# Kernel optimization log

Hardware: AMD Instinct MI355X
Metric: run time of the kernel (lower is better)

The kernel has to match this reference:

```python
import jax, jax.numpy as jnp
import numpy as np
import math

B, N, WIDTH, HEADS = 2, 2048, 1024, 16
ATTN_CH = WIDTH // HEADS  # 64 (note: width//heads//3 of the 3*width fused dim)


def setup_inputs() -> dict:
    key = jax.random.key(0)
    ks = jax.random.split(key, 3)
    std = 0.02
    return {
        "x": jax.random.normal(ks[0], (B, N, WIDTH), dtype=jnp.float32),
        "w_qkv": jax.random.normal(ks[1], (WIDTH, 3 * WIDTH), dtype=jnp.float32) * std,
        "b_qkv": jnp.zeros((3 * WIDTH,), dtype=jnp.float32),
        "w_proj": jax.random.normal(ks[2], (WIDTH, WIDTH), dtype=jnp.float32) * std,
        "b_proj": jnp.zeros((WIDTH,), dtype=jnp.float32),
    }


def reference(x, w_qkv, b_qkv, w_proj, b_proj):
    bs, n_ctx, width = x.shape
    qkv = x @ w_qkv + b_qkv                       # [b, n, 3*width]
    attn_ch = (3 * width) // HEADS // 3           # head dim
    scale = 1.0 / math.sqrt(math.sqrt(attn_ch))
    # per-head layout: [b, n, heads, 3*attn_ch] -> split q,k,v
    qkv = qkv.reshape(bs, n_ctx, HEADS, 3 * attn_ch)
    q, k, v = jnp.split(qkv, 3, axis=-1)          # each [b, n, h, c]
    weight = jnp.einsum("bthc,bshc->bhts", q * scale, k * scale)
    weight = jax.nn.softmax(weight.astype(jnp.float32), axis=-1).astype(qkv.dtype)
    out = jnp.einsum("bhts,bshc->bthc", weight, v).reshape(bs, n_ctx, -1)
    return out @ w_proj + b_proj
```

## Files before the change

### kernel.cpp

```cpp
#include <hip/hip_runtime.h>
#include <hip/hip_fp16.h>

#define BATCH 2
#define NCTX  2048
#define WIDTH 1024
#define HEADS 16
#define CH    64
#define QKVD  (3 * WIDTH)
#define MROWS (BATCH * NCTX)

typedef __attribute__((ext_vector_type(4))) float    f32x4;
typedef __attribute__((ext_vector_type(8))) _Float16 f16x8;
typedef __attribute__((ext_vector_type(4))) _Float16 f16x4;

#define QSCALE 0.18033688011112042f

__device__ __forceinline__ unsigned pkrtz(float a, float b) {
    auto p = __builtin_amdgcn_cvt_pkrtz(a, b);
    return __builtin_bit_cast(unsigned, p);
}

__global__ __launch_bounds__(256)
void split_x_f16(const float* __restrict__ x, __half* __restrict__ tiles)
{
    const int mb = blockIdx.x, kt = blockIdx.y;
    const int t = threadIdx.x;
    __half* tb = (__half*)tiles + ((size_t)mb * 32 + kt) * 4096;
    #pragma unroll
    for (int it = 0; it < 2; ++it) {
        const int idx = it * 256 + t;
        const int m = idx >> 2, q = idx & 3;
        const float* src = x + (size_t)(mb * 128 + m) * WIDTH + kt * 32 + q * 8;
        const f32x4 v0 = *(const f32x4*)src;
        const f32x4 v1 = *(const f32x4*)(src + 4);
        f16x8 h;
        #pragma unroll
        for (int j = 0; j < 4; ++j) { h[j] = (_Float16)v0[j]; h[4 + j] = (_Float16)v1[j]; }
        *(f16x8*)&tb[(q * 128 + m) * 8] = h;
    }
}

__global__ __launch_bounds__(256)
void split_w_f16(const float* __restrict__ w, __half* __restrict__ tiles, int N)
{
    __shared__ float tile[32][129];
    const int nb = blockIdx.x, kt = blockIdx.y;
    const int t = threadIdx.x;
    #pragma unroll
    for (int it = 0; it < 2; ++it) {
        const int idx = it * 256 + t;
        const int kk = idx >> 4, n8 = idx & 15;
        const float* src = w + (size_t)(kt * 32 + kk) * N + nb * 128 + n8 * 8;
        #pragma unroll
        for (int j = 0; j < 8; ++j) tile[kk][n8 * 8 + j] = src[j];
    }
    __syncthreads();
    __half* tb = tiles + ((size_t)nb * 32 + kt) * 4096;
    #pragma unroll
    for (int it = 0; it < 2; ++it) {
        const int idx = it * 256 + t;
        const int q = idx >> 7, nn = idx & 127;
        f16x8 h;
        #pragma unroll
        for (int j = 0; j < 8; ++j) h[j] = (_Float16)tile[q * 8 + j][nn];
        *(f16x8*)&tb[(q * 128 + nn) * 8] = h;
    }
}

__global__ __launch_bounds__(256)
void gemm_qkv(const __half* __restrict__ At, const __half* __restrict__ Bt,
              const float* __restrict__ bias,
              __half* __restrict__ qg, __half* __restrict__ kg, __half* __restrict__ vtg)
{
    __shared__ __align__(16) _Float16 sm[16384];
    const int t = threadIdx.x, lane = t & 63, w = t >> 6;
    const int lq = lane & 15, quad = lane >> 4;
    const int nb = blockIdx.x, mb = blockIdx.y;
    const int wm = (w >> 1) * 64, wn = (w & 1) * 64;

    const __half* Ab = At + ((size_t)mb * 32) * 4096;
    const __half* Bb = Bt + ((size_t)nb * 32) * 4096;
    const int c0 = w * 4;

    f32x4 acc[4][4];
    #pragma unroll
    for (int i = 0; i < 4; ++i)
        #pragma unroll
        for (int j = 0; j < 4; ++j) acc[i][j] = 0;

    f16x8 pf[4];
    #pragma unroll
    for (int i = 0; i < 4; ++i) {
        const int c = c0 + i;
        const __half* g = (c < 8 ? Ab + c * 512 : Bb + (c - 8) * 512) + lane * 8;
        pf[i] = *(const f16x8*)g;
    }
    #pragma unroll
    for (int i = 0; i < 4; ++i)
        *(f16x8*)&sm[(c0 + i) * 512 + lane * 8] = pf[i];
    __syncthreads();

    for (int kt = 0; kt < 32; ++kt) {
        _Float16* cur = sm + (kt & 1) * 8192;

        if (kt + 1 < 32) {
            #pragma unroll
            for (int i = 0; i < 4; ++i) {
                const int c = c0 + i;
                const __half* g = (c < 8 ? Ab + (size_t)(kt + 1) * 4096 + c * 512
                                         : Bb + (size_t)(kt + 1) * 4096 + (c - 8) * 512) + lane * 8;
                pf[i] = *(const f16x8*)g;
            }
        }

        f16x8 a[4], b[4];
        #pragma unroll
        for (int i = 0; i < 4; ++i) {
            a[i] = *(const f16x8*)&cur[(quad * 128 + wm + i * 16 + lq) * 8];
            b[i] = *(const f16x8*)&cur[4096 + (quad * 128 + wn + i * 16 + lq) * 8];
        }
        #pragma unroll
        for (int i = 0; i < 4; ++i)
            #pragma unroll
            for (int j = 0; j < 4; ++j)
                acc[i][j] = __builtin_amdgcn_mfma_f32_16x16x32_f16(a[i], b[j], acc[i][j], 0, 0, 0);

        if (kt + 1 < 32) {
            #pragma unroll
            for (int i = 0; i < 4; ++i)
                *(f16x8*)&sm[((kt + 1) & 1) * 8192 + (c0 + i) * 512 + lane * 8] = pf[i];
        }
        __syncthreads();
    }

    const int bb = mb >> 4;
    #pragma unroll
    for (int jf = 0; jf < 4; ++jf) {
        const int col = nb * 128 + wn + jf * 16 + lq;
        const int h = col / 192;
        const int sect = col - h * 192;
        const int type = sect >> 6;
        const int c = sect & 63;
        const float bv = bias[col];
        const size_t bh = (size_t)bb * 16 + h;
        #pragma unroll
        for (int i = 0; i < 4; ++i) {
            #pragma unroll
            for (int r = 0; r < 4; ++r) {
                const int n = (mb & 15) * 128 + wm + i * 16 + quad * 4 + r;
                const float v = acc[i][jf][r] + bv;
                if (type == 0) {
                    const size_t a2 = ((bh * 16 + (n >> 7)) * 8 + (c >> 3)) * 1024
                                      + (size_t)(n & 127) * 8 + (c & 7);
                    qg[a2] = __float2half(v * QSCALE);
                } else if (type == 1) {
                    const size_t a2 = ((bh * 32 + (n >> 6)) * 8 + (c >> 3)) * 512
                                      + (size_t)(n & 63) * 8 + (c & 7);
                    kg[a2] = __float2half(v);
                } else {
                    const size_t a2 = ((bh * 32 + (n >> 6)) * 8 + ((n >> 3) & 7)) * 512
                                      + (size_t)c * 8 + (n & 7);
                    vtg[a2] = __float2half(v);
                }
            }
        }
    }
}

__global__ __launch_bounds__(256, 2)
void attn_mfma10(const __half* __restrict__ qg, const __half* __restrict__ kg,
                 const __half* __restrict__ vtg, __half* __restrict__ a2)
{
    __shared__ __align__(16) float red[4][3][2][16][16];
    __shared__ __align__(16) float rol2[4][4][16];

    const int t = threadIdx.x, lane = t & 63, w = t >> 6;
    const int lq = lane & 15, quad = lane >> 4;
    const int bid = blockIdx.x;
    const int qt = (bid >> 3) & 31;
    const int bh_ = (bid & 7) + ((bid >> 8) << 3);
    const size_t bh = (size_t)bh_;
    const int h = bh_ & 15, b = bh_ >> 4;

    const __half* qtile = qg + (bh * 16 + (qt >> 1)) * 8192;
    const __half* kbase = kg + bh * 32 * 4096;
    const __half* vbase = vtg + bh * 32 * 4096;

    const int qrow0 = (qt & 1) * 64;
    f16x8 aq[4][2];
    #pragma unroll
    for (int qn = 0; qn < 4; ++qn)
        #pragma unroll
        for (int ks = 0; ks < 2; ++ks)
            aq[qn][ks] = *(const f16x8*)(qtile + (size_t)(ks * 4 + quad) * 1024
                                         + (qrow0 + qn * 16 + lq) * 8);

    const int kofs0 = ((0 * 4 + quad) * 64 + w * 16 + lq) * 8;
    const int kofs1 = ((1 * 4 + quad) * 64 + w * 16 + lq) * 8;
    int vofs[4];
    #pragma unroll
    for (int jc = 0; jc < 4; ++jc)
        vofs[jc] = ((w * 2 + (quad >> 1)) * 64 + jc * 16 + lq) * 8 + (quad & 1) * 4;

    f32x4 O[4][4];
    float ls[4];
    #pragma unroll
    for (int qn = 0; qn < 4; ++qn) {
        ls[qn] = 0.0f;
        #pragma unroll
        for (int jc = 0; jc < 4; ++jc) O[qn][jc] = 0;
    }
    const f32x4 zc = {0.0f, 0.0f, 0.0f, 0.0f};

    f16x8 kf0 = *(const f16x8*)(kbase + kofs0);
    f16x8 kf1 = *(const f16x8*)(kbase + kofs1);
    f16x4 vf[4];
    #pragma unroll
    for (int jc = 0; jc < 4; ++jc) vf[jc] = *(const f16x4*)(vbase + vofs[jc]);

    const __half* kp = kbase + 4096;
    const __half* vp = vbase + 4096;

    for (int kt = 0; kt < 32; ++kt) {
        f16x8 kn0, kn1; f16x4 vn[4];
        if (kt < 31) {
            kn0 = *(const f16x8*)(kp + kofs0);
            kn1 = *(const f16x8*)(kp + kofs1);
            #pragma unroll
            for (int jc = 0; jc < 4; ++jc) vn[jc] = *(const f16x4*)(vp + vofs[jc]);
            kp += 4096; vp += 4096;
        }

        __builtin_amdgcn_s_setprio(1);
        #pragma unroll
        for (int qn = 0; qn < 4; ++qn) {
            f32x4 st = __builtin_amdgcn_mfma_f32_16x16x32_f16(kf0, aq[qn][0], zc, 0, 0, 0);
            st = __builtin_amdgcn_mfma_f32_16x16x32_f16(kf1, aq[qn][1], st, 0, 0, 0);
            const float e0 = __builtin_amdgcn_exp2f(st[0]);
            const float e1 = __builtin_amdgcn_exp2f(st[1]);
            const float e2 = __builtin_amdgcn_exp2f(st[2]);
            const float e3 = __builtin_amdgcn_exp2f(st[3]);
            ls[qn] += (e0 + e1) + (e2 + e3);
            uint2 pk;
            pk.x = pkrtz(e0, e1);
            pk.y = pkrtz(e2, e3);
            const f16x4 pa = __builtin_bit_cast(f16x4, pk);
            #pragma unroll
            for (int jc = 0; jc < 4; ++jc)
                O[qn][jc] = __builtin_amdgcn_mfma_f32_16x16x16f16(pa, vf[jc], O[qn][jc], 0, 0, 0);
        }
        __builtin_amdgcn_s_setprio(0);

        if (kt < 31) {
            kf0 = kn0; kf1 = kn1;
            #pragma unroll
            for (int jc = 0; jc < 4; ++jc) vf[jc] = vn[jc];
        }
    }

    float lsw[4];
    #pragma unroll
    for (int qn = 0; qn < 4; ++qn) {
        float v = ls[qn];
        v += __shfl_xor(v, 16, 64);
        v += __shfl_xor(v, 32, 64);
        lsw[qn] = v;
    }

    #pragma unroll
    for (int qn = 0; qn < 4; ++qn) {
        if (quad == 0)
            rol2[qn][w][lq] = lsw[qn];
        if (qn != w) {
            const int rel = (w < qn) ? w : w - 1;
            *(f32x4*)&red[qn][rel][0][lq][quad * 4] = O[qn][0];
            *(f32x4*)&red[qn][rel][1][lq][quad * 4] = O[qn][1];
        }
    }
    __syncthreads();

    float linv[4];
    f32x4 s0 = zc, s1 = zc;
    #pragma unroll
    for (int qn = 0; qn < 4; ++qn) {
        if (qn == w) {
            f32x4 lt = zc;
            #pragma unroll
            for (int w2 = 0; w2 < 4; ++w2)
                lt += *(const f32x4*)&rol2[qn][w2][quad * 4];
            #pragma unroll
            for (int r = 0; r < 4; ++r) linv[r] = 1.0f / lt[r];
            s0 = O[qn][0];
            s1 = O[qn][1];
            #pragma unroll
            for (int src = 0; src < 3; ++src) {
                s0 += *(const f32x4*)&red[qn][src][0][lq][quad * 4];
                s1 += *(const f32x4*)&red[qn][src][1][lq][quad * 4];
            }
        }
    }

    __half* a2t = a2 + ((size_t)(b * 16 + (qt >> 1)) * 32) * 4096;
    const int mb0 = (qt & 1) * 64 + w * 16 + quad * 4;

    {
        const int ch0 = h * 64 + 0 * 16 + lq;
        const int ktp0 = ch0 >> 5, qc0 = (ch0 >> 3) & 3, j0 = ch0 & 7;
        #pragma unroll
        for (int r = 0; r < 4; ++r)
            a2t[(size_t)ktp0 * 4096 + (qc0 * 128 + mb0 + r) * 8 + j0] =
                __float2half(s0[r] * linv[r]);
        const int ch1 = h * 64 + 1 * 16 + lq;
        const int ktp1 = ch1 >> 5, qc1 = (ch1 >> 3) & 3, j1 = ch1 & 7;
        #pragma unroll
        for (int r = 0; r < 4; ++r)
            a2t[(size_t)ktp1 * 4096 + (qc1 * 128 + mb0 + r) * 8 + j1] =
                __float2half(s1[r] * linv[r]);
    }
    __syncthreads();

    #pragma unroll
    for (int qn = 0; qn < 4; ++qn) {
        if (qn != w) {
            const int rel = (w < qn) ? w : w - 1;
            *(f32x4*)&red[qn][rel][0][lq][quad * 4] = O[qn][2];
            *(f32x4*)&red[qn][rel][1][lq][quad * 4] = O[qn][3];
        }
    }
    __syncthreads();

    f32x4 s2 = zc, s3 = zc;
    #pragma unroll
    for (int qn = 0; qn < 4; ++qn) {
        if (qn == w) {
            s2 = O[qn][2];
            s3 = O[qn][3];
            #pragma unroll
            for (int src = 0; src < 3; ++src) {
                s2 += *(const f32x4*)&red[qn][src][0][lq][quad * 4];
                s3 += *(const f32x4*)&red[qn][src][1][lq][quad * 4];
            }
        }
    }

    {
        const int ch2 = h * 64 + 2 * 16 + lq;
        const int ktp2 = ch2 >> 5, qc2 = (ch2 >> 3) & 3, j2 = ch2 & 7;
        #pragma unroll
        for (int r = 0; r < 4; ++r)
            a2t[(size_t)ktp2 * 4096 + (qc2 * 128 + mb0 + r) * 8 + j2] =
                __float2half(s2[r] * linv[r]);
        const int ch3 = h * 64 + 3 * 16 + lq;
        const int ktp3 = ch3 >> 5, qc3 = (ch3 >> 3) & 3, j3 = ch3 & 7;
        #pragma unroll
        for (int r = 0; r < 4; ++r)
            a2t[(size_t)ktp3 * 4096 + (qc3 * 128 + mb0 + r) * 8 + j3] =
                __float2half(s3[r] * linv[r]);
    }
}

__global__ __launch_bounds__(256)
void gemm_proj(const __half* __restrict__ At, const __half* __restrict__ Bt,
               const float* __restrict__ bias, float* __restrict__ out)
{
    __shared__ __align__(16) _Float16 sm[16384];
    const int t = threadIdx.x, lane = t & 63, w = t >> 6;
    const int lq = lane & 15, quad = lane >> 4;
    const int nb = blockIdx.x, mb = blockIdx.y;
    const int wm = (w >> 1) * 64, wn = (w & 1) * 64;

    const __half* Ab = At + ((size_t)mb * 32) * 4096;
    const __half* Bb = Bt + ((size_t)nb * 32) * 4096;
    const int c0 = w * 4;

    f32x4 acc[4][4];
    #pragma unroll
    for (int i = 0; i < 4; ++i)
        #pragma unroll
        for (int j = 0; j < 4; ++j) acc[i][j] = 0;

    f16x8 pf[4];
    #pragma unroll
    for (int i = 0; i < 4; ++i) {
        const int c = c0 + i;
        const __half* g = (c < 8 ? Ab + c * 512 : Bb + (c - 8) * 512) + lane * 8;
        pf[i] = *(const f16x8*)g;
    }
    #pragma unroll
    for (int i = 0; i < 4; ++i)
        *(f16x8*)&sm[(c0 + i) * 512 + lane * 8] = pf[i];
    __syncthreads();

    for (int kt = 0; kt < 32; ++kt) {
        _Float16* cur = sm + (kt & 1) * 8192;

        if (kt + 1 < 32) {
            #pragma unroll
            for (int i = 0; i < 4; ++i) {
                const int c = c0 + i;
                const __half* g = (c < 8 ? Ab + (size_t)(kt + 1) * 4096 + c * 512
                                         : Bb + (size_t)(kt + 1) * 4096 + (c - 8) * 512) + lane * 8;
                pf[i] = *(const f16x8*)g;
            }
        }

        f16x8 a[4], b[4];
        #pragma unroll
        for (int i = 0; i < 4; ++i) {
            a[i] = *(const f16x8*)&cur[(quad * 128 + wm + i * 16 + lq) * 8];
            b[i] = *(const f16x8*)&cur[4096 + (quad * 128 + wn + i * 16 + lq) * 8];
        }
        #pragma unroll
        for (int i = 0; i < 4; ++i)
            #pragma unroll
            for (int j = 0; j < 4; ++j)
                acc[i][j] = __builtin_amdgcn_mfma_f32_16x16x32_f16(a[i], b[j], acc[i][j], 0, 0, 0);

        if (kt + 1 < 32) {
            #pragma unroll
            for (int i = 0; i < 4; ++i)
                *(f16x8*)&sm[((kt + 1) & 1) * 8192 + (c0 + i) * 512 + lane * 8] = pf[i];
        }
        __syncthreads();
    }

    #pragma unroll
    for (int jf = 0; jf < 4; ++jf) {
        const int col = nb * 128 + wn + jf * 16 + lq;
        const float bv = bias[col];
        #pragma unroll
        for (int i = 0; i < 4; ++i)
            #pragma unroll
            for (int r = 0; r < 4; ++r) {
                const int row = mb * 128 + wm + i * 16 + quad * 4 + r;
                out[(size_t)row * WIDTH + col] = acc[i][jf][r] + bv;
            }
    }
}

extern "C" void kernel_launch(void* const* d_in, const int* in_sizes, int n_in,
                              void* d_out, int out_size, void* d_ws, size_t ws_size,
                              hipStream_t stream)
{
    const float* x      = (const float*)d_in[0];
    const float* w_qkv  = (const float*)d_in[1];
    const float* b_qkv  = (const float*)d_in[2];
    const float* w_proj = (const float*)d_in[3];
    const float* b_proj = (const float*)d_in[4];
    float* out = (float*)d_out;

    char* p = (char*)d_ws;
    size_t o = 0;
    __half* A1  = (__half*)(p + o); o += (size_t)MROWS * WIDTH * 2;
    __half* Bq  = (__half*)(p + o); o += (size_t)WIDTH * QKVD * 2;
    __half* Qg  = (__half*)(p + o); o += (size_t)MROWS * WIDTH * 2;
    __half* Kg  = (__half*)(p + o); o += (size_t)MROWS * WIDTH * 2;
    __half* Vtg = (__half*)(p + o); o += (size_t)MROWS * WIDTH * 2;
    __half* A2  = (__half*)(p + o); o += (size_t)MROWS * WIDTH * 2;
    __half* Bp  = (__half*)(p + o); o += (size_t)WIDTH * WIDTH * 2;

    dim3 blk(256);

    split_x_f16<<<dim3(32, 32), blk, 0, stream>>>(x, A1);
    split_w_f16<<<dim3(24, 32), blk, 0, stream>>>(w_qkv, Bq, QKVD);
    split_w_f16<<<dim3(8, 32),  blk, 0, stream>>>(w_proj, Bp, WIDTH);

    gemm_qkv<<<dim3(24, 32), blk, 0, stream>>>(A1, Bq, b_qkv, Qg, Kg, Vtg);

    attn_mfma10<<<dim3(1024), blk, 0, stream>>>(Qg, Kg, Vtg, A2);

    gemm_proj<<<dim3(8, 32), blk, 0, stream>>>(A2, Bp, b_proj, out);
}
```

Before: 191.5 us.

## Halve attention query tile to 32 rows per block and raise occupancy

Each attention block now handles 32 query rows instead of 64, doubling the grid to 2048 blocks and raising the launch-bounds occupancy hint from 2 to 4 blocks per CU. Fewer accumulators per thread cut register pressure, and the cross-wave reduction is redone so each wave finalizes a 16-row by 32-channel slice in one shared-memory pass instead of two. The cost is that K and V tiles are read from global memory by twice as many blocks, which doubles that traffic per query.

```diff
diff --git a/kernel.cpp b/kernel.cpp
--- a/kernel.cpp
+++ b/kernel.cpp
@@ -167,29 +167,29 @@
     }
 }
 
-__global__ __launch_bounds__(256, 2)
-void attn_mfma10(const __half* __restrict__ qg, const __half* __restrict__ kg,
+__global__ __launch_bounds__(256, 4)
+void attn_mfma11(const __half* __restrict__ qg, const __half* __restrict__ kg,
                  const __half* __restrict__ vtg, __half* __restrict__ a2)
 {
-    __shared__ __align__(16) float red[4][3][2][16][16];
-    __shared__ __align__(16) float rol2[4][4][16];
+    __shared__ __align__(16) float red[2][2][3][2][16][16];
+    __shared__ __align__(16) float rol2[2][4][16];
 
     const int t = threadIdx.x, lane = t & 63, w = t >> 6;
     const int lq = lane & 15, quad = lane >> 4;
     const int bid = blockIdx.x;
-    const int qt = (bid >> 3) & 31;
-    const int bh_ = (bid & 7) + ((bid >> 8) << 3);
+    const int qt = (bid >> 3) & 63;
+    const int bh_ = (bid & 7) + ((bid >> 9) << 3);
     const size_t bh = (size_t)bh_;
     const int h = bh_ & 15, b = bh_ >> 4;
 
-    const __half* qtile = qg + (bh * 16 + (qt >> 1)) * 8192;
+    const __half* qtile = qg + (bh * 16 + (qt >> 2)) * 8192;
     const __half* kbase = kg + bh * 32 * 4096;
     const __half* vbase = vtg + bh * 32 * 4096;
 
-    const int qrow0 = (qt & 1) * 64;
-    f16x8 aq[4][2];
-    #pragma unroll
-    for (int qn = 0; qn < 4; ++qn)
+    const int qrow0 = (qt & 3) * 32;
+    f16x8 aq[2][2];
+    #pragma unroll
+    for (int qn = 0; qn < 2; ++qn)
         #pragma unroll
         for (int ks = 0; ks < 2; ++ks)
             aq[qn][ks] = *(const f16x8*)(qtile + (size_t)(ks * 4 + quad) * 1024
@@ -202,10 +202,10 @@
     for (int jc = 0; jc < 4; ++jc)
         vofs[jc] = ((w * 2 + (quad >> 1)) * 64 + jc * 16 + lq) * 8 + (quad & 1) * 4;
 
-    f32x4 O[4][4];
-    float ls[4];
-    #pragma unroll
-    for (int qn = 0; qn < 4; ++qn) {
+    f32x4 O[2][4];
+    float ls[2];
+    #pragma unroll
+    for (int qn = 0; qn < 2; ++qn) {
         ls[qn] = 0.0f;
         #pragma unroll
         for (int jc = 0; jc < 4; ++jc) O[qn][jc] = 0;
@@ -233,7 +233,7 @@
 
         __builtin_amdgcn_s_setprio(1);
         #pragma unroll
-        for (int qn = 0; qn < 4; ++qn) {
+        for (int qn = 0; qn < 2; ++qn) {
             f32x4 st = __builtin_amdgcn_mfma_f32_16x16x32_f16(kf0, aq[qn][0], zc, 0, 0, 0);
             st = __builtin_amdgcn_mfma_f32_16x16x32_f16(kf1, aq[qn][1], st, 0, 0, 0);
             const float e0 = __builtin_amdgcn_exp2f(st[0]);
@@ -258,9 +258,9 @@
         }
     }
 
-    float lsw[4];
-    #pragma unroll
-    for (int qn = 0; qn < 4; ++qn) {
+    float lsw[2];
+    #pragma unroll
+    for (int qn = 0; qn < 2; ++qn) {
         float v = ls[qn];
         v += __shfl_xor(v, 16, 64);
         v += __shfl_xor(v, 32, 64);
@@ -268,13 +268,17 @@
     }
 
     #pragma unroll
-    for (int qn = 0; qn < 4; ++qn) {
+    for (int t2 = 0; t2 < 2; ++t2) {
         if (quad == 0)
-            rol2[qn][w][lq] = lsw[qn];
-        if (qn != w) {
-            const int rel = (w < qn) ? w : w - 1;
-            *(f32x4*)&red[qn][rel][0][lq][quad * 4] = O[qn][0];
-            *(f32x4*)&red[qn][rel][1][lq][quad * 4] = O[qn][1];
+            rol2[t2][w][lq] = lsw[t2];
+        #pragma unroll
+        for (int p = 0; p < 2; ++p) {
+            const int ow = t2 * 2 + p;
+            if (ow != w) {
+                const int rel = (w < ow) ? w : w - 1;
+                *(f32x4*)&red[t2][p][rel][0][lq][quad * 4] = O[t2][p * 2];
+                *(f32x4*)&red[t2][p][rel][1][lq][quad * 4] = O[t2][p * 2 + 1];
+            }
         }
     }
     __syncthreads();
@@ -282,80 +286,44 @@
     float linv[4];
     f32x4 s0 = zc, s1 = zc;
     #pragma unroll
-    for (int qn = 0; qn < 4; ++qn) {
-        if (qn == w) {
-            f32x4 lt = zc;
-            #pragma unroll
-            for (int w2 = 0; w2 < 4; ++w2)
-                lt += *(const f32x4*)&rol2[qn][w2][quad * 4];
-            #pragma unroll
-            for (int r = 0; r < 4; ++r) linv[r] = 1.0f / lt[r];
-            s0 = O[qn][0];
-            s1 = O[qn][1];
-            #pragma unroll
-            for (int src = 0; src < 3; ++src) {
-                s0 += *(const f32x4*)&red[qn][src][0][lq][quad * 4];
-                s1 += *(const f32x4*)&red[qn][src][1][lq][quad * 4];
-            }
-        }
-    }
-
-    __half* a2t = a2 + ((size_t)(b * 16 + (qt >> 1)) * 32) * 4096;
-    const int mb0 = (qt & 1) * 64 + w * 16 + quad * 4;
+    for (int t2 = 0; t2 < 2; ++t2) {
+        #pragma unroll
+        for (int p = 0; p < 2; ++p) {
+            if (t2 * 2 + p == w) {
+                f32x4 lt = zc;
+                #pragma unroll
+                for (int w2 = 0; w2 < 4; ++w2)
+                    lt += *(const f32x4*)&rol2[t2][w2][quad * 4];
+                #pragma unroll
+                for (int r = 0; r < 4; ++r) linv[r] = 1.0f / lt[r];
+                s0 = O[t2][p * 2];
+                s1 = O[t2][p * 2 + 1];
+                #pragma unroll
+                for (int src = 0; src < 3; ++src) {
+                    s0 += *(const f32x4*)&red[t2][p][src][0][lq][quad * 4];
+                    s1 += *(const f32x4*)&red[t2][p][src][1][lq][quad * 4];
+                }
+            }
+        }
+    }
+
+    __half* a2t = a2 + ((size_t)(b * 16 + (qt >> 2)) * 32) * 4096;
+    const int mb0 = (qt & 3) * 32 + (w >> 1) * 16 + quad * 4;
+    const int jc0 = (w & 1) * 2;
 
     {
-        const int ch0 = h * 64 + 0 * 16 + lq;
+        const int ch0 = h * 64 + (jc0 + 0) * 16 + lq;
         const int ktp0 = ch0 >> 5, qc0 = (ch0 >> 3) & 3, j0 = ch0 & 7;
         #pragma unroll
         for (int r = 0; r < 4; ++r)
             a2t[(size_t)ktp0 * 4096 + (qc0 * 128 + mb0 + r) * 8 + j0] =
                 __float2half(s0[r] * linv[r]);
-        const int ch1 = h * 64 + 1 * 16 + lq;
+        const int ch1 = h * 64 + (jc0 + 1) * 16 + lq;
         const int ktp1 = ch1 >> 5, qc1 = (ch1 >> 3) & 3, j1 = ch1 & 7;
         #pragma unroll
         for (int r = 0; r < 4; ++r)
             a2t[(size_t)ktp1 * 4096 + (qc1 * 128 + mb0 + r) * 8 + j1] =
                 __float2half(s1[r] * linv[r]);
-    }
-    __syncthreads();
-
-    #pragma unroll
-    for (int qn = 0; qn < 4; ++qn) {
-        if (qn != w) {
-            const int rel = (w < qn) ? w : w - 1;
-            *(f32x4*)&red[qn][rel][0][lq][quad * 4] = O[qn][2];
-            *(f32x4*)&red[qn][rel][1][lq][quad * 4] = O[qn][3];
-        }
-    }
-    __syncthreads();
-
-    f32x4 s2 = zc, s3 = zc;
-    #pragma unroll
-    for (int qn = 0; qn < 4; ++qn) {
-        if (qn == w) {
-            s2 = O[qn][2];
-            s3 = O[qn][3];
-            #pragma unroll
-            for (int src = 0; src < 3; ++src) {
-                s2 += *(const f32x4*)&red[qn][src][0][lq][quad * 4];
-                s3 += *(const f32x4*)&red[qn][src][1][lq][quad * 4];
-            }
-        }
-    }
-
-    {
-        const int ch2 = h * 64 + 2 * 16 + lq;
-        const int ktp2 = ch2 >> 5, qc2 = (ch2 >> 3) & 3, j2 = ch2 & 7;
-        #pragma unroll
-        for (int r = 0; r < 4; ++r)
-            a2t[(size_t)ktp2 * 4096 + (qc2 * 128 + mb0 + r) * 8 + j2] =
-                __float2half(s2[r] * linv[r]);
-        const int ch3 = h * 64 + 3 * 16 + lq;
-        const int ktp3 = ch3 >> 5, qc3 = (ch3 >> 3) & 3, j3 = ch3 & 7;
-        #pragma unroll
-        for (int r = 0; r < 4; ++r)
-            a2t[(size_t)ktp3 * 4096 + (qc3 * 128 + mb0 + r) * 8 + j3] =
-                __float2half(s3[r] * linv[r]);
     }
 }
 
@@ -467,7 +435,7 @@
 
     gemm_qkv<<<dim3(24, 32), blk, 0, stream>>>(A1, Bq, b_qkv, Qg, Kg, Vtg);
 
-    attn_mfma10<<<dim3(1024), blk, 0, stream>>>(Qg, Kg, Vtg, A2);
+    attn_mfma11<<<dim3(2048), blk, 0, stream>>>(Qg, Kg, Vtg, A2);
 
     gemm_proj<<<dim3(8, 32), blk, 0, stream>>>(A2, Bp, b_proj, out);
 }
```

Measured after the change: 203.5 us. +6.3%, slower.

## Merge fp16 conversion kernels into one launch and widen gemm_proj to eight waves

Applied to the files above, without the earlier changes.

The three separate fp32-to-fp16 tiling kernels (x, w_qkv, w_proj) are combined into one kernel that picks its job from the block index, removing two kernel launches and their gaps. gemm_proj now runs 512 threads per block, with eight waves each computing a 64x32 sub-tile instead of four waves each computing 64x64. This halves per-wave accumulators and global prefetch work and puts more waves on each CU, since only 256 blocks exist. The trade-off is less register-level reuse of the B fragments per MFMA and more threads waiting at each per-iteration barrier.

```diff
diff --git a/kernel.cpp b/kernel.cpp
--- a/kernel.cpp
+++ b/kernel.cpp
@@ -21,31 +21,41 @@
 }
 
 __global__ __launch_bounds__(256)
-void split_x_f16(const float* __restrict__ x, __half* __restrict__ tiles)
-{
-    const int mb = blockIdx.x, kt = blockIdx.y;
-    const int t = threadIdx.x;
-    __half* tb = (__half*)tiles + ((size_t)mb * 32 + kt) * 4096;
-    #pragma unroll
-    for (int it = 0; it < 2; ++it) {
-        const int idx = it * 256 + t;
-        const int m = idx >> 2, q = idx & 3;
-        const float* src = x + (size_t)(mb * 128 + m) * WIDTH + kt * 32 + q * 8;
-        const f32x4 v0 = *(const f32x4*)src;
-        const f32x4 v1 = *(const f32x4*)(src + 4);
-        f16x8 h;
-        #pragma unroll
-        for (int j = 0; j < 4; ++j) { h[j] = (_Float16)v0[j]; h[4 + j] = (_Float16)v1[j]; }
-        *(f16x8*)&tb[(q * 128 + m) * 8] = h;
-    }
-}
-
-__global__ __launch_bounds__(256)
-void split_w_f16(const float* __restrict__ w, __half* __restrict__ tiles, int N)
+void split_all(const float* __restrict__ x,
+               const float* __restrict__ w_qkv, const float* __restrict__ w_proj,
+               __half* __restrict__ A1, __half* __restrict__ Bq, __half* __restrict__ Bp)
 {
     __shared__ float tile[32][129];
-    const int nb = blockIdx.x, kt = blockIdx.y;
+    const int bid = blockIdx.x;
     const int t = threadIdx.x;
+
+    if (bid < 1024) {
+        const int mb = bid >> 5, kt = bid & 31;
+        __half* tb = A1 + ((size_t)mb * 32 + kt) * 4096;
+        #pragma unroll
+        for (int it = 0; it < 2; ++it) {
+            const int idx = it * 256 + t;
+            const int m = idx >> 2, q = idx & 3;
+            const float* src = x + (size_t)(mb * 128 + m) * WIDTH + kt * 32 + q * 8;
+            const f32x4 v0 = *(const f32x4*)src;
+            const f32x4 v1 = *(const f32x4*)(src + 4);
+            f16x8 h;
+            #pragma unroll
+            for (int j = 0; j < 4; ++j) { h[j] = (_Float16)v0[j]; h[4 + j] = (_Float16)v1[j]; }
+            *(f16x8*)&tb[(q * 128 + m) * 8] = h;
+        }
+        return;
+    }
+
+    const float* w; __half* tiles; int N, nb, kt;
+    if (bid < 1792) {
+        const int u = bid - 1024;
+        w = w_qkv; tiles = Bq; N = QKVD; nb = u >> 5; kt = u & 31;
+    } else {
+        const int u = bid - 1792;
+        w = w_proj; tiles = Bp; N = WIDTH; nb = u >> 5; kt = u & 31;
+    }
+
     #pragma unroll
     for (int it = 0; it < 2; ++it) {
         const int idx = it * 256 + t;
@@ -359,7 +369,7 @@
     }
 }
 
-__global__ __launch_bounds__(256)
+__global__ __launch_bounds__(512)
 void gemm_proj(const __half* __restrict__ At, const __half* __restrict__ Bt,
                const float* __restrict__ bias, float* __restrict__ out)
 {
@@ -367,27 +377,27 @@
     const int t = threadIdx.x, lane = t & 63, w = t >> 6;
     const int lq = lane & 15, quad = lane >> 4;
     const int nb = blockIdx.x, mb = blockIdx.y;
-    const int wm = (w >> 1) * 64, wn = (w & 1) * 64;
+    const int wm = (w >> 2) * 64, wn = (w & 3) * 32;
 
     const __half* Ab = At + ((size_t)mb * 32) * 4096;
     const __half* Bb = Bt + ((size_t)nb * 32) * 4096;
-    const int c0 = w * 4;
-
-    f32x4 acc[4][4];
+    const int c0 = w * 2;
+
+    f32x4 acc[4][2];
     #pragma unroll
     for (int i = 0; i < 4; ++i)
         #pragma unroll
-        for (int j = 0; j < 4; ++j) acc[i][j] = 0;
-
-    f16x8 pf[4];
-    #pragma unroll
-    for (int i = 0; i < 4; ++i) {
+        for (int j = 0; j < 2; ++j) acc[i][j] = 0;
+
+    f16x8 pf[2];
+    #pragma unroll
+    for (int i = 0; i < 2; ++i) {
         const int c = c0 + i;
         const __half* g = (c < 8 ? Ab + c * 512 : Bb + (c - 8) * 512) + lane * 8;
         pf[i] = *(const f16x8*)g;
     }
     #pragma unroll
-    for (int i = 0; i < 4; ++i)
+    for (int i = 0; i < 2; ++i)
         *(f16x8*)&sm[(c0 + i) * 512 + lane * 8] = pf[i];
     __syncthreads();
 
@@ -396,7 +406,7 @@
 
         if (kt + 1 < 32) {
             #pragma unroll
-            for (int i = 0; i < 4; ++i) {
+            for (int i = 0; i < 2; ++i) {
                 const int c = c0 + i;
                 const __half* g = (c < 8 ? Ab + (size_t)(kt + 1) * 4096 + c * 512
                                          : Bb + (size_t)(kt + 1) * 4096 + (c - 8) * 512) + lane * 8;
@@ -404,28 +414,29 @@
             }
         }
 
-        f16x8 a[4], b[4];
-        #pragma unroll
-        for (int i = 0; i < 4; ++i) {
+        f16x8 a[4], b[2];
+        #pragma unroll
+        for (int i = 0; i < 4; ++i)
             a[i] = *(const f16x8*)&cur[(quad * 128 + wm + i * 16 + lq) * 8];
-            b[i] = *(const f16x8*)&cur[4096 + (quad * 128 + wn + i * 16 + lq) * 8];
-        }
+        #pragma unroll
+        for (int j = 0; j < 2; ++j)
+            b[j] = *(const f16x8*)&cur[4096 + (quad * 128 + wn + j * 16 + lq) * 8];
         #pragma unroll
         for (int i = 0; i < 4; ++i)
             #pragma unroll
-            for (int j = 0; j < 4; ++j)
+            for (int j = 0; j < 2; ++j)
                 acc[i][j] = __builtin_amdgcn_mfma_f32_16x16x32_f16(a[i], b[j], acc[i][j], 0, 0, 0);
 
         if (kt + 1 < 32) {
             #pragma unroll
-            for (int i = 0; i < 4; ++i)
+            for (int i = 0; i < 2; ++i)
                 *(f16x8*)&sm[((kt + 1) & 1) * 8192 + (c0 + i) * 512 + lane * 8] = pf[i];
         }
         __syncthreads();
     }
 
     #pragma unroll
-    for (int jf = 0; jf < 4; ++jf) {
+    for (int jf = 0; jf < 2; ++jf) {
         const int col = nb * 128 + wn + jf * 16 + lq;
         const float bv = bias[col];
         #pragma unroll
@@ -459,15 +470,11 @@
     __half* A2  = (__half*)(p + o); o += (size_t)MROWS * WIDTH * 2;
     __half* Bp  = (__half*)(p + o); o += (size_t)WIDTH * WIDTH * 2;
 
-    dim3 blk(256);
-
-    split_x_f16<<<dim3(32, 32), blk, 0, stream>>>(x, A1);
-    split_w_f16<<<dim3(24, 32), blk, 0, stream>>>(w_qkv, Bq, QKVD);
-    split_w_f16<<<dim3(8, 32),  blk, 0, stream>>>(w_proj, Bp, WIDTH);
-
-    gemm_qkv<<<dim3(24, 32), blk, 0, stream>>>(A1, Bq, b_qkv, Qg, Kg, Vtg);
-
-    attn_mfma10<<<dim3(1024), blk, 0, stream>>>(Qg, Kg, Vtg, A2);
-
-    gemm_proj<<<dim3(8, 32), blk, 0, stream>>>(A2, Bp, b_proj, out);
-}
+    split_all<<<dim3(2048), dim3(256), 0, stream>>>(x, w_qkv, w_proj, A1, Bq, Bp);
+
+    gemm_qkv<<<dim3(24, 32), dim3(256), 0, stream>>>(A1, Bq, b_qkv, Qg, Kg, Vtg);
+
+    attn_mfma10<<<dim3(1024), dim3(256), 0, stream>>>(Qg, Kg, Vtg, A2);
+
+    gemm_proj<<<dim3(8, 32), dim3(512), 0, stream>>>(A2, Bp, b_proj, out);
+}
```

Result: no change. 194.9 us (+1.7%).
